# Performance work log

Measured on AMD Instinct MI355X. Metric: run time of the kernel, lower is better.

The kernel has to match this reference:

```python
import jax, jax.numpy as jnp
import numpy as np

EXP_SCALE = 10.0   # self.exp_param_scale
BETA_UP = 5.0      # self.kernel_beta_upbound
N_HEAD = 12


def setup_inputs() -> dict:
    key = jax.random.key(0)
    ks = jax.random.split(key, 7)
    B, T, C, nh = 2, 2048, 768, N_HEAD
    s = 1.0 / np.sqrt(C)
    x = jax.random.normal(ks[0], (B, T, C), jnp.float32)
    W_la = jax.random.normal(ks[1], (C, C), jnp.float32) * s      # LeakyAverage linear
    la_coef = jax.random.uniform(ks[2], (nh,), jnp.float32)        # per-head leaky decay in (0,1)
    W_v = jax.random.normal(ks[3], (C, C), jnp.float32) * s        # v_featurizer linear
    v_coef = jax.random.uniform(ks[4], (nh,), jnp.float32)         # v_featurizer per-head coef
    kernel_beta = jnp.ones((nh,), jnp.float32) / EXP_SCALE
    value_beta = jnp.ones((nh,), jnp.float32) * (-0.5 / EXP_SCALE)
    W_proj = jax.random.normal(ks[5], (C, C), jnp.float32) * s     # c_proj
    return dict(x=x, W_la=W_la, la_coef=la_coef, W_v=W_v, v_coef=v_coef,
                kernel_beta=kernel_beta, value_beta=value_beta, W_proj=W_proj)


def _leaky_average(x, W_la, la_coef):
    # y_t = c * y_{t-1} + (1-c) * (x W^T)_t, per-head decay c. Returns (B, nh, T, hs).
    B, T, C = x.shape
    nh = la_coef.shape[0]
    hs = C // nh
    u = (x @ W_la.T).reshape(B, T, nh, hs)
    c = la_coef[None, :, None]  # (1, nh, 1) broadcast over (B, nh, hs)

    def step(carry, ut):
        y = c * carry + (1.0 - c) * ut
        return y, y

    _, ys = jax.lax.scan(step, jnp.zeros((B, nh, hs), x.dtype), jnp.swapaxes(u, 0, 1))
    return jnp.transpose(ys, (1, 2, 0, 3))  # (T,B,nh,hs) -> (B,nh,T,hs)


def reference(x, W_la, la_coef, W_v, v_coef, kernel_beta, value_beta, W_proj):
    B, T, C = x.shape
    nh = la_coef.shape[0]
    hs = C // nh
    v_shift = 1

    # K path: leaky-average features, L2-normalize, exp-kernel beta scale
    k0 = _leaky_average(x, W_la, la_coef)                               # (B,nh,T,hs)
    raw_k = k0 / (jnp.linalg.norm(k0, axis=-1, keepdims=True) + 1e-6)
    beta = jnp.exp(jnp.minimum(kernel_beta * EXP_SCALE, BETA_UP))
    k = raw_k * beta[None, :, None, None]

    # V path: lowrlinearconv featurizer (linear, shift-by-1 mix, normalize) + value scale
    xl = (x @ W_v.T).reshape(B, T, nh, hs).transpose(0, 2, 1, 3)        # (B,nh,T,hs)
    shifted = jnp.concatenate([xl[:, :, 1:], jnp.zeros_like(xl[:, :, :1])], axis=2)
    vc = v_coef[None, :, None, None]
    vf = shifted * (1.0 - vc) + xl * vc
    vf = vf / (jnp.linalg.norm(vf, axis=-1, keepdims=True) + 1e-6)
    vbeta = jnp.exp(jnp.minimum(value_beta * EXP_SCALE, BETA_UP))
    v = vf * vbeta[None, :, None, None]

    # shifted-causal attention: query at position t (t>=1) attends keys 0..t-1, scale=1.0
    q = k[:, :, v_shift:]                                               # (B,nh,T-1,hs)
    scores = jnp.einsum('bhqd,bhkd->bhqk', q, k)                        # (B,nh,T-1,T)
    mask = jnp.tril(jnp.ones((T - v_shift, T), bool))                   # j <= iq  <=>  key < query pos
    scores = jnp.where(mask, scores, -jnp.inf)
    attn = jax.nn.softmax(scores, axis=-1)
    o = jnp.einsum('bhqk,bhkd->bhqd', attn, v)
    y = jnp.concatenate([jnp.zeros((B, nh, v_shift, hs), x.dtype), o], axis=2)

    y = y.transpose(0, 2, 1, 3).reshape(B, T, C)
    return y @ W_proj.T  # c_proj (dropouts are identity in eval)
```

## Files before the change

### kernel.cpp

```cpp
#include <hip/hip_runtime.h>
#include <hip/hip_bf16.h>
#include <math.h>

#define B_   2
#define T_   2048
#define C_   768
#define NH   12
#define HS   64
#define NSEG 64
#define SEGLEN 32
#define CX   1536

typedef __attribute__((ext_vector_type(8))) short short8;
typedef __attribute__((ext_vector_type(4))) short short4v;
typedef __attribute__((ext_vector_type(4))) float f32x4;

static __device__ inline unsigned short f2b(float f) {
  __hip_bfloat16 h = __float2bfloat16(f);
  unsigned short u;
  __builtin_memcpy(&u, &h, 2);
  return u;
}

#define GLOAD_LDS16(gp, lp)                                                        \
  __builtin_amdgcn_global_load_lds((const __attribute__((address_space(1))) void*)(gp), \
                                   (__attribute__((address_space(3))) void*)(lp), 16, 0, 0)

__global__ __launch_bounds__(256) void cast_all(const float* __restrict__ x,
                                                const float* __restrict__ wla,
                                                const float* __restrict__ wv,
                                                const float* __restrict__ wp,
                                                __hip_bfloat16* __restrict__ xb,
                                                __hip_bfloat16* __restrict__ wcat,
                                                __hip_bfloat16* __restrict__ wpb) {
  const int NX4 = (B_ * T_ * C_) / 4;
  const int NW4 = (C_ * C_) / 4;
  const int TOT = NX4 + 3 * NW4;
  int i = blockIdx.x * 256 + threadIdx.x;
  int st = gridDim.x * 256;
  for (; i < TOT; i += st) {
    const float* s;
    unsigned short* d;
    if (i < NX4) { s = x + (size_t)i * 4; d = (unsigned short*)xb + (size_t)i * 4; }
    else if (i < NX4 + NW4) { int j = i - NX4; s = wla + (size_t)j * 4; d = (unsigned short*)wcat + (size_t)j * 4; }
    else if (i < NX4 + 2 * NW4) { int j = i - NX4 - NW4; s = wv + (size_t)j * 4; d = (unsigned short*)wcat + (size_t)(C_ * C_) + (size_t)j * 4; }
    else { int j = i - NX4 - 2 * NW4; s = wp + (size_t)j * 4; d = (unsigned short*)wpb + (size_t)j * 4; }
    float4 v = *(const float4*)s;
    short4v o;
    o.x = (short)f2b(v.x); o.y = (short)f2b(v.y); o.z = (short)f2b(v.z); o.w = (short)f2b(v.w);
    *(short4v*)d = o;
  }
}

template <int BM>
__global__ __launch_bounds__(256) void gemm_bf16(const __hip_bfloat16* __restrict__ A,
                                                 const __hip_bfloat16* __restrict__ Bw,
                                                 float* __restrict__ C,
                                                 int M, int N, int K) {
  __shared__ __hip_bfloat16 As[BM * 64];
  __shared__ __hip_bfloat16 Bs[128 * 64];
  const int tid = threadIdx.x;
  const int w = tid >> 6, lane = tid & 63;
  const int bm = blockIdx.x * BM, bn = blockIdx.y * 128;
  const int q16 = lane & 15, lg = lane >> 4;

  constexpr int NACC = (BM == 128) ? 4 : 2;
  f32x4 acc[4][NACC];
#pragma unroll
  for (int i = 0; i < 4; ++i)
#pragma unroll
    for (int j = 0; j < NACC; ++j) acc[i][j] = (f32x4){0.f, 0.f, 0.f, 0.f};

  const int srow = (lane >> 3);
  const int soff0 = (lane & 7) * 16;
  const int sw = (lane & 7) << 4;
  constexpr int ACH = BM / 8;
  constexpr int CPW = (ACH + 16) / 4;

  for (int k0 = 0; k0 < K; k0 += 64) {
    __syncthreads();
#pragma unroll
    for (int c = 0; c < CPW; ++c) {
      int gc = w * CPW + c;
      int isB = gc >= ACH;
      int ci = isB ? gc - ACH : gc;
      int row = ci * 8 + srow;
      int soff = soff0 ^ ((row & 7) << 4);
      const __hip_bfloat16* gp =
          (isB ? Bw + (size_t)(bn + row) * K : A + (size_t)(bm + row) * K) + k0 + (soff >> 1);
      __hip_bfloat16* lp = (isB ? Bs : As) + ci * 512;
      GLOAD_LDS16(gp, lp);
    }
    __syncthreads();
#pragma unroll
    for (int ks = 0; ks < 2; ++ks) {
      short8 af[4], bf[NACC];
      const int colb = ks * 64 + lg * 16;
#pragma unroll
      for (int i = 0; i < 4; ++i) {
        int ra = (BM == 128) ? ((w >> 1) * 64 + i * 16 + q16) : (i * 16 + q16);
        af[i] = *(const short8*)((const char*)As + ra * 128 + (colb ^ sw));
      }
#pragma unroll
      for (int j = 0; j < NACC; ++j) {
        int rb = (BM == 128) ? ((w & 1) * 64 + j * 16 + q16) : (w * 32 + j * 16 + q16);
        bf[j] = *(const short8*)((const char*)Bs + rb * 128 + (colb ^ sw));
      }
#pragma unroll
      for (int i = 0; i < 4; ++i)
#pragma unroll
        for (int j = 0; j < NACC; ++j)
          acc[i][j] = __builtin_amdgcn_mfma_f32_16x16x32_bf16(af[i], bf[j], acc[i][j], 0, 0, 0);
    }
  }
#pragma unroll
  for (int i = 0; i < 4; ++i) {
#pragma unroll
    for (int r = 0; r < 4; ++r) {
      int m = (BM == 128) ? (bm + (w >> 1) * 64 + i * 16 + lg * 4 + r)
                          : (bm + i * 16 + lg * 4 + r);
      int nb = (BM == 128) ? (bn + (w & 1) * 64 + q16) : (bn + w * 32 + q16);
      float* cp = C + (size_t)m * N + nb;
#pragma unroll
      for (int j = 0; j < NACC; ++j) cp[j * 16] = acc[i][j][r];
    }
  }
}

__global__ __launch_bounds__(256) void scan_seg(const float* __restrict__ uxv,
                                                const float* __restrict__ la_coef,
                                                float* __restrict__ segend) {
  int cid = blockIdx.x * 4 + (threadIdx.x >> 6);
  int d   = threadIdx.x & 63;
  int seg = cid & (NSEG - 1);
  int bh  = cid >> 6;
  int h   = bh % NH;
  int b   = bh / NH;
  float c  = la_coef[h];
  float oc = 1.f - c;
  int t0 = seg * SEGLEN;
  const float* up = uxv + ((size_t)b * T_ + t0) * CX + h * HS + d;
  float y = 0.f;
  for (int i = 0; i < SEGLEN; ++i)
    y = fmaf(c, y, oc * up[(size_t)i * CX]);
  segend[(size_t)cid * HS + d] = y;
}

__global__ __launch_bounds__(256) void scan_b(const float* __restrict__ la_coef,
                                              const float* __restrict__ segend,
                                              float* __restrict__ carryin) {
  int s = blockIdx.x * 256 + threadIdx.x;
  if (s >= B_ * NH * HS) return;
  int d  = s & 63;
  int bh = s >> 6;
  int h  = bh % NH;
  float c = la_coef[h];
  float cl = c;
#pragma unroll
  for (int i = 0; i < 5; ++i) cl *= cl;
  float h0 = 0.f;
  for (int seg = 0; seg < NSEG; ++seg) {
    int cid = bh * NSEG + seg;
    carryin[(size_t)cid * HS + d] = h0;
    h0 = fmaf(cl, h0, segend[(size_t)cid * HS + d]);
  }
}

__global__ __launch_bounds__(256) void scan_c_norm(const float* __restrict__ la_coef,
                                                   const float* __restrict__ kernel_beta,
                                                   const float* __restrict__ carryin,
                                                   const float* __restrict__ uxv,
                                                   __hip_bfloat16* __restrict__ kb16) {
  int cid = blockIdx.x * 4 + (threadIdx.x >> 6);
  int d   = threadIdx.x & 63;
  int seg = cid & (NSEG - 1);
  int bh  = cid >> 6;
  int h   = bh % NH;
  int b   = bh / NH;
  float c  = la_coef[h];
  float oc = 1.f - c;
  float bk = __expf(fminf(kernel_beta[h] * 10.f, 5.f));
  int t0 = seg * SEGLEN;
  const float* up = uxv + ((size_t)b * T_ + t0) * CX + h * HS + d;
  __hip_bfloat16* op = kb16 + ((size_t)bh * T_ + t0) * HS + d;
  float y = carryin[(size_t)cid * HS + d];
  for (int i = 0; i < SEGLEN; ++i) {
    y = fmaf(c, y, oc * up[(size_t)i * CX]);
    float ss = y * y;
#pragma unroll
    for (int off = 1; off < 64; off <<= 1) ss += __shfl_xor(ss, off, 64);
    float scale = bk / (sqrtf(ss) + 1e-6f);
    op[(size_t)i * HS] = __float2bfloat16(y * scale);
  }
}

__global__ __launch_bounds__(256) void vbuild_t(const float* __restrict__ uxv,
                                                const float* __restrict__ v_coef,
                                                const float* __restrict__ value_beta,
                                                __hip_bfloat16* __restrict__ vt) {
  __shared__ __hip_bfloat16 sm[64][73];
  int t0 = blockIdx.x * 64;
  int bh = blockIdx.y;
  int h = bh % NH, b = bh / NH;
  int w = threadIdx.x >> 6, lane = threadIdx.x & 63;
  float vc = v_coef[h];
  float vb = __expf(fminf(value_beta[h] * 10.f, 5.f));
  for (int i = 0; i < 16; ++i) {
    int tl = w * 16 + i;
    int t = t0 + tl;
    const float* xp = uxv + ((size_t)b * T_ + t) * CX + 768 + h * HS + lane;
    float x0 = *xp;
    float x1 = (t + 1 < T_) ? xp[CX] : 0.f;
    float vf = (1.f - vc) * x1 + vc * x0;
    float ss = vf * vf;
#pragma unroll
    for (int off = 1; off < 64; off <<= 1) ss += __shfl_xor(ss, off, 64);
    sm[tl][lane] = __float2bfloat16(vf * vb / (sqrtf(ss) + 1e-6f));
  }
  __syncthreads();
  int d = threadIdx.x >> 3;
  int c = threadIdx.x & 7;
  for (int i = 0; i < 2; ++i) {
    int dd = d + i * 32;
    short8 v;
#pragma unroll
    for (int k = 0; k < 8; ++k)
      v[k] = (short)((const unsigned short*)&sm[c * 8 + k][dd])[0];
    *(short8*)((unsigned short*)vt + ((size_t)bh * HS + dd) * T_ + t0 + c * 8) = v;
  }
}

__global__ __launch_bounds__(256, 3) void attn6(const __hip_bfloat16* __restrict__ Kg,
                                                const __hip_bfloat16* __restrict__ Vtg,
                                                const float* __restrict__ kernel_beta,
                                                __hip_bfloat16* __restrict__ Y) {
  __shared__ __hip_bfloat16 Kt[2][64 * 64];
  __shared__ __hip_bfloat16 Vt[2][64 * 64];
  __shared__ char Pl[4][2304];
  const int bh = blockIdx.x;
  const int b = bh / NH, h = bh % NH;
  const int w = threadIdx.x >> 6, lane = threadIdx.x & 63;
  const int q16 = lane & 15, lg = lane >> 4;
  const int it = 31 - blockIdx.y;
  const int qb0 = 1 + it * 64;
  float bk = __expf(fminf(kernel_beta[h] * 10.f, 5.f));
  float m0 = bk * bk;
  const unsigned short* Kh = (const unsigned short*)Kg + (size_t)bh * T_ * HS;
  const unsigned short* Vh = (const unsigned short*)Vtg + (size_t)bh * HS * T_;
  unsigned short* Yh = (unsigned short*)Y + (size_t)b * T_ * C_ + h * HS;

  if (it == 0 && w == 0) Yh[lane] = 0;

  const int tq = qb0 + w * 16 + q16;
  short8 qf[2];
  {
    int tqc = tq > T_ - 1 ? T_ - 1 : tq;
#pragma unroll
    for (int ks = 0; ks < 2; ++ks)
      qf[ks] = *(const short8*)(Kh + (size_t)tqc * HS + ks * 32 + lg * 8);
  }

  f32x4 zero = {0.f, 0.f, 0.f, 0.f};
  f32x4 accO[4];
#pragma unroll
  for (int mt = 0; mt < 4; ++mt) accO[mt] = zero;
  float lsum = 0.f;

  char* pb = &Pl[w][0] + q16 * 144;
  const int swr = (q16 & 7) << 4;

  const int srow = lane >> 3;
  const int soff = ((lane & 7) << 4) ^ (srow << 4);

  const int NT = (qb0 + 126) >> 6;

#define STAGE_KV(buf, j0)                                                             \
  {                                                                                   \
    _Pragma("unroll")                                                                 \
    for (int n = 0; n < 2; ++n) {                                                     \
      int ch = w * 2 + n;                                                             \
      int row = ch * 8 + srow;                                                        \
      GLOAD_LDS16((const char*)(Kh + (size_t)((j0) + row) * HS) + soff,               \
                  &Kt[buf][ch * 512]);                                                \
      GLOAD_LDS16((const char*)(Vh + (size_t)row * T_ + (j0)) + soff,                 \
                  &Vt[buf][ch * 512]);                                                \
    }                                                                                 \
  }

  STAGE_KV(0, 0);

  for (int kt = 0; kt < NT; ++kt) {
    const int cur = kt & 1;
    const int j0 = kt * 64;
    if (kt + 1 < NT) {
      STAGE_KV(cur ^ 1, j0 + 64);
      asm volatile("s_waitcnt vmcnt(4)" ::: "memory");
    } else {
      asm volatile("s_waitcnt vmcnt(0)" ::: "memory");
    }
    __builtin_amdgcn_s_barrier();
    __builtin_amdgcn_sched_barrier(0);

    const char* Kb = (const char*)&Kt[cur][0];
    const char* Vb = (const char*)&Vt[cur][0];
    short8 kf[4][2], vf[4][2];
#pragma unroll
    for (int nt = 0; nt < 4; ++nt)
#pragma unroll
      for (int ks = 0; ks < 2; ++ks) {
        const int colb = ks * 64 + lg * 16;
        kf[nt][ks] = *(const short8*)(Kb + (nt * 16 + q16) * 128 + (colb ^ swr));
        vf[nt][ks] = *(const short8*)(Vb + (nt * 16 + q16) * 128 + (colb ^ swr));
      }
    f32x4 s[4];
    __builtin_amdgcn_s_setprio(1);
#pragma unroll
    for (int nt = 0; nt < 4; ++nt) {
      s[nt] = __builtin_amdgcn_mfma_f32_16x16x32_bf16(kf[nt][0], qf[0], zero, 0, 0, 0);
      s[nt] = __builtin_amdgcn_mfma_f32_16x16x32_bf16(kf[nt][1], qf[1], s[nt], 0, 0, 0);
    }
    __builtin_amdgcn_s_setprio(0);
#pragma unroll
    for (int nt = 0; nt < 4; ++nt) {
      float p[4];
#pragma unroll
      for (int r = 0; r < 4; ++r) {
        int j = j0 + nt * 16 + lg * 4 + r;
        p[r] = (j < tq) ? __expf(s[nt][r] - m0) : 0.f;
        lsum += p[r];
      }
      unsigned int w0, w1;
      asm("v_cvt_pk_bf16_f32 %0, %1, %2" : "=v"(w0) : "v"(p[0]), "v"(p[1]));
      asm("v_cvt_pk_bf16_f32 %0, %1, %2" : "=v"(w1) : "v"(p[2]), "v"(p[3]));
      uint2 pk; pk.x = w0; pk.y = w1;
      *(uint2*)(pb + nt * 32 + lg * 8) = pk;
    }
    __builtin_amdgcn_s_setprio(1);
#pragma unroll
    for (int ks = 0; ks < 2; ++ks) {
      short8 pf = *(const short8*)(pb + ks * 64 + lg * 16);
#pragma unroll
      for (int mt = 0; mt < 4; ++mt)
        accO[mt] = __builtin_amdgcn_mfma_f32_16x16x32_bf16(vf[mt][ks], pf, accO[mt], 0, 0, 0);
    }
    __builtin_amdgcn_s_setprio(0);
    asm volatile("s_waitcnt lgkmcnt(0)" ::: "memory");
    __builtin_amdgcn_s_barrier();
  }

  {
    float v = lsum;
    v += __shfl_xor(v, 16, 64);
    v += __shfl_xor(v, 32, 64);
    float inv = 1.f / v;
    if (tq < T_) {
      unsigned short* yp = Yh + (size_t)tq * C_;
#pragma unroll
      for (int mt = 0; mt < 4; ++mt) {
        float o0 = accO[mt][0] * inv, o1 = accO[mt][1] * inv;
        float o2 = accO[mt][2] * inv, o3 = accO[mt][3] * inv;
        unsigned int u0, u1;
        asm("v_cvt_pk_bf16_f32 %0, %1, %2" : "=v"(u0) : "v"(o0), "v"(o1));
        asm("v_cvt_pk_bf16_f32 %0, %1, %2" : "=v"(u1) : "v"(o2), "v"(o3));
        uint2 pk; pk.x = u0; pk.y = u1;
        *(uint2*)(yp + mt * 16 + lg * 4) = pk;
      }
    }
  }
#undef STAGE_KV
}

extern "C" void kernel_launch(void* const* d_in, const int* in_sizes, int n_in,
                              void* d_out, int out_size, void* d_ws, size_t ws_size,
                              hipStream_t stream) {
  const float* x          = (const float*)d_in[0];
  const float* W_la       = (const float*)d_in[1];
  const float* la_coef    = (const float*)d_in[2];
  const float* W_v        = (const float*)d_in[3];
  const float* v_coef     = (const float*)d_in[4];
  const float* kernel_bet = (const float*)d_in[5];
  const float* value_bet  = (const float*)d_in[6];
  const float* W_proj     = (const float*)d_in[7];
  float* out = (float*)d_out;

  float* ws = (float*)d_ws;
  const size_t NTOK = (size_t)B_ * T_ * C_;
  const size_t NSEGTOT = (size_t)B_ * NH * NSEG * HS;
  float* uxv     = ws;
  float* segend  = uxv + (size_t)B_ * T_ * CX;
  float* carryin = segend + NSEGTOT;
  __hip_bfloat16* kb16 = (__hip_bfloat16*)(carryin + NSEGTOT);
  __hip_bfloat16* vt16 = kb16 + NTOK;
  __hip_bfloat16* xb   = vt16 + NTOK;
  __hip_bfloat16* Wcat = xb + NTOK;
  __hip_bfloat16* Wpb  = Wcat + (size_t)CX * C_;
  __hip_bfloat16* yb   = xb;

  const int M = B_ * T_;

  cast_all<<<2048, 256, 0, stream>>>(x, W_la, W_v, W_proj, xb, Wcat, Wpb);

  gemm_bf16<128><<<dim3(M / 128, CX / 128), 256, 0, stream>>>(xb, Wcat, uxv, M, CX, C_);

  scan_seg<<<dim3(B_ * NH * NSEG / 4), 256, 0, stream>>>(uxv, la_coef, segend);
  scan_b<<<dim3((B_ * NH * HS + 255) / 256), 256, 0, stream>>>(la_coef, segend, carryin);
  scan_c_norm<<<dim3(B_ * NH * NSEG / 4), 256, 0, stream>>>(la_coef, kernel_bet, carryin, uxv, kb16);

  vbuild_t<<<dim3(T_ / 64, B_ * NH), 256, 0, stream>>>(uxv, v_coef, value_bet, vt16);

  attn6<<<dim3(B_ * NH, 32), 256, 0, stream>>>(kb16, vt16, kernel_bet, yb);

  gemm_bf16<64><<<dim3(M / 64, C_ / 128), 256, 0, stream>>>(yb, Wpb, out, M, C_, C_);
}
```

Baseline: 112.4 us.

## Software-pipeline attention so QK of tile k overlaps softmax/PV of tile k-1

```diff
diff --git a/kernel.cpp b/kernel.cpp
--- a/kernel.cpp
+++ b/kernel.cpp
@@ -230,12 +230,12 @@
   }
 }
 
-__global__ __launch_bounds__(256, 3) void attn6(const __hip_bfloat16* __restrict__ Kg,
+__global__ __launch_bounds__(256, 4) void attn7(const __hip_bfloat16* __restrict__ Kg,
                                                 const __hip_bfloat16* __restrict__ Vtg,
                                                 const float* __restrict__ kernel_beta,
                                                 __hip_bfloat16* __restrict__ Y) {
   __shared__ __hip_bfloat16 Kt[2][64 * 64];
-  __shared__ __hip_bfloat16 Vt[2][64 * 64];
+  __shared__ __hip_bfloat16 Vt[3][64 * 64];
   __shared__ char Pl[4][2304];
   const int bh = blockIdx.x;
   const int b = bh / NH, h = bh % NH;
@@ -265,6 +265,7 @@
 #pragma unroll
   for (int mt = 0; mt < 4; ++mt) accO[mt] = zero;
   float lsum = 0.f;
+  f32x4 sp[4];
 
   char* pb = &Pl[w][0] + q16 * 144;
   const int swr = (q16 & 7) << 4;
@@ -274,26 +275,58 @@
 
   const int NT = (qb0 + 126) >> 6;
 
-#define STAGE_KV(buf, j0)                                                             \
+#define STAGE_KV(kbuf, vbuf, j0)                                                      \
   {                                                                                   \
     _Pragma("unroll")                                                                 \
     for (int n = 0; n < 2; ++n) {                                                     \
       int ch = w * 2 + n;                                                             \
       int row = ch * 8 + srow;                                                        \
       GLOAD_LDS16((const char*)(Kh + (size_t)((j0) + row) * HS) + soff,               \
-                  &Kt[buf][ch * 512]);                                                \
+                  &Kt[kbuf][ch * 512]);                                               \
       GLOAD_LDS16((const char*)(Vh + (size_t)row * T_ + (j0)) + soff,                 \
-                  &Vt[buf][ch * 512]);                                                \
+                  &Vt[vbuf][ch * 512]);                                               \
     }                                                                                 \
   }
 
-  STAGE_KV(0, 0);
+#define SM_PV(tp)                                                                     \
+  {                                                                                   \
+    const int j0p = (tp)*64;                                                          \
+    const char* Vb = (const char*)&Vt[(tp) % 3][0];                                   \
+    _Pragma("unroll")                                                                 \
+    for (int nt = 0; nt < 4; ++nt) {                                                  \
+      float p[4];                                                                     \
+      _Pragma("unroll")                                                               \
+      for (int r = 0; r < 4; ++r) {                                                   \
+        int j = j0p + nt * 16 + lg * 4 + r;                                           \
+        p[r] = (j < tq) ? __expf(sp[nt][r] - m0) : 0.f;                               \
+        lsum += p[r];                                                                 \
+      }                                                                               \
+      unsigned int w0, w1;                                                            \
+      asm("v_cvt_pk_bf16_f32 %0, %1, %2" : "=v"(w0) : "v"(p[0]), "v"(p[1]));          \
+      asm("v_cvt_pk_bf16_f32 %0, %1, %2" : "=v"(w1) : "v"(p[2]), "v"(p[3]));          \
+      uint2 pk; pk.x = w0; pk.y = w1;                                                 \
+      *(uint2*)(pb + nt * 32 + lg * 8) = pk;                                          \
+    }                                                                                 \
+    __builtin_amdgcn_s_setprio(1);                                                    \
+    _Pragma("unroll")                                                                 \
+    for (int ks = 0; ks < 2; ++ks) {                                                  \
+      short8 pf = *(const short8*)(pb + ks * 64 + lg * 16);                           \
+      _Pragma("unroll")                                                               \
+      for (int mt = 0; mt < 4; ++mt) {                                                \
+        short8 vf = *(const short8*)(Vb + (mt * 16 + q16) * 128 +                     \
+                                     ((ks * 64 + lg * 16) ^ swr));                    \
+        accO[mt] = __builtin_amdgcn_mfma_f32_16x16x32_bf16(vf, pf, accO[mt], 0, 0, 0);\
+      }                                                                               \
+    }                                                                                 \
+    __builtin_amdgcn_s_setprio(0);                                                    \
+  }
+
+  STAGE_KV(0, 0, 0);
 
   for (int kt = 0; kt < NT; ++kt) {
-    const int cur = kt & 1;
     const int j0 = kt * 64;
     if (kt + 1 < NT) {
-      STAGE_KV(cur ^ 1, j0 + 64);
+      STAGE_KV((kt + 1) & 1, (kt + 1) % 3, j0 + 64);
       asm volatile("s_waitcnt vmcnt(4)" ::: "memory");
     } else {
       asm volatile("s_waitcnt vmcnt(0)" ::: "memory");
@@ -301,52 +334,31 @@
     __builtin_amdgcn_s_barrier();
     __builtin_amdgcn_sched_barrier(0);
 
-    const char* Kb = (const char*)&Kt[cur][0];
-    const char* Vb = (const char*)&Vt[cur][0];
-    short8 kf[4][2], vf[4][2];
+    const char* Kb = (const char*)&Kt[kt & 1][0];
+    short8 kf[4][2];
 #pragma unroll
     for (int nt = 0; nt < 4; ++nt)
 #pragma unroll
-      for (int ks = 0; ks < 2; ++ks) {
-        const int colb = ks * 64 + lg * 16;
-        kf[nt][ks] = *(const short8*)(Kb + (nt * 16 + q16) * 128 + (colb ^ swr));
-        vf[nt][ks] = *(const short8*)(Vb + (nt * 16 + q16) * 128 + (colb ^ swr));
-      }
-    f32x4 s[4];
+      for (int ks = 0; ks < 2; ++ks)
+        kf[nt][ks] = *(const short8*)(Kb + (nt * 16 + q16) * 128 + ((ks * 64 + lg * 16) ^ swr));
+    f32x4 sc[4];
     __builtin_amdgcn_s_setprio(1);
 #pragma unroll
     for (int nt = 0; nt < 4; ++nt) {
-      s[nt] = __builtin_amdgcn_mfma_f32_16x16x32_bf16(kf[nt][0], qf[0], zero, 0, 0, 0);
-      s[nt] = __builtin_amdgcn_mfma_f32_16x16x32_bf16(kf[nt][1], qf[1], s[nt], 0, 0, 0);
+      sc[nt] = __builtin_amdgcn_mfma_f32_16x16x32_bf16(kf[nt][0], qf[0], zero, 0, 0, 0);
+      sc[nt] = __builtin_amdgcn_mfma_f32_16x16x32_bf16(kf[nt][1], qf[1], sc[nt], 0, 0, 0);
     }
     __builtin_amdgcn_s_setprio(0);
-#pragma unroll
-    for (int nt = 0; nt < 4; ++nt) {
-      float p[4];
-#pragma unroll
-      for (int r = 0; r < 4; ++r) {
-        int j = j0 + nt * 16 + lg * 4 + r;
-        p[r] = (j < tq) ? __expf(s[nt][r] - m0) : 0.f;
-        lsum += p[r];
-      }
-      unsigned int w0, w1;
-      asm("v_cvt_pk_bf16_f32 %0, %1, %2" : "=v"(w0) : "v"(p[0]), "v"(p[1]));
-      asm("v_cvt_pk_bf16_f32 %0, %1, %2" : "=v"(w1) : "v"(p[2]), "v"(p[3]));
-      uint2 pk; pk.x = w0; pk.y = w1;
-      *(uint2*)(pb + nt * 32 + lg * 8) = pk;
-    }
-    __builtin_amdgcn_s_setprio(1);
-#pragma unroll
-    for (int ks = 0; ks < 2; ++ks) {
-      short8 pf = *(const short8*)(pb + ks * 64 + lg * 16);
-#pragma unroll
-      for (int mt = 0; mt < 4; ++mt)
-        accO[mt] = __builtin_amdgcn_mfma_f32_16x16x32_bf16(vf[mt][ks], pf, accO[mt], 0, 0, 0);
-    }
-    __builtin_amdgcn_s_setprio(0);
+
+    if (kt > 0) SM_PV(kt - 1);
+
+#pragma unroll
+    for (int nt = 0; nt < 4; ++nt) sp[nt] = sc[nt];
+
     asm volatile("s_waitcnt lgkmcnt(0)" ::: "memory");
     __builtin_amdgcn_s_barrier();
   }
+  SM_PV(NT - 1);
 
   {
     float v = lsum;
@@ -368,6 +380,7 @@
     }
   }
 #undef STAGE_KV
+#undef SM_PV
 }
 
 extern "C" void kernel_launch(void* const* d_in, const int* in_sizes, int n_in,
@@ -400,7 +413,7 @@
 
   cast_all<<<2048, 256, 0, stream>>>(x, W_la, W_v, W_proj, xb, Wcat, Wpb);
 
-  gemm_bf16<128><<<dim3(M / 128, CX / 128), 256, 0, stream>>>(xb, Wcat, uxv, M, CX, C_);
+  gemm_bf16<64><<<dim3(M / 64, CX / 128), 256, 0, stream>>>(xb, Wcat, uxv, M, CX, C_);
 
   scan_seg<<<dim3(B_ * NH * NSEG / 4), 256, 0, stream>>>(uxv, la_coef, segend);
   scan_b<<<dim3((B_ * NH * HS + 255) / 256), 256, 0, stream>>>(la_coef, segend, carryin);
@@ -408,7 +421,7 @@
 
   vbuild_t<<<dim3(T_ / 64, B_ * NH), 256, 0, stream>>>(uxv, v_coef, value_bet, vt16);
 
-  attn6<<<dim3(B_ * NH, 32), 256, 0, stream>>>(kb16, vt16, kernel_bet, yb);
+  attn7<<<dim3(B_ * NH, 32), 256, 0, stream>>>(kb16, vt16, kernel_bet, yb);
 
   gemm_bf16<64><<<dim3(M / 64, C_ / 128), 256, 0, stream>>>(yb, Wpb, out, M, C_, C_);
 }
```

Result: no change. 110.7 us (-1.5%).
